# Kernel tuning notes

Hardware: AMD Instinct MI355X
Metric: run time of the kernel (lower is better)

## Reference

```python
import jax, jax.numpy as jnp
import numpy as np

B, S, D = 1024, 200, 512
D_FF = 256


def setup_inputs() -> dict:
    key = jax.random.key(0)
    ks = jax.random.split(key, 8)
    s = 0.02  # init scale to keep gates in a sane range
    return {
        "target": jax.random.normal(ks[0], (B, D), jnp.float32),
        "history": jax.random.normal(ks[1], (B, S, D), jnp.float32),
        "W_ih": jax.random.normal(ks[2], (3 * D, D), jnp.float32) * s,
        "W_hh": jax.random.normal(ks[3], (3 * D, D), jnp.float32) * s,
        "b_ih": jnp.zeros((3 * D,), jnp.float32),
        "b_hh": jnp.zeros((3 * D,), jnp.float32),
        "W_fc": jax.random.normal(ks[4], (D_FF, 2 * D), jnp.float32) * s,
        "b_fc": jnp.zeros((D_FF,), jnp.float32),
        "W_sc": jax.random.normal(ks[5], (1, D_FF), jnp.float32) * s,
        "b_sc": jnp.zeros((1,), jnp.float32),
    }


def _gru(history, W_ih, W_hh, b_ih, b_hh):
    # Precompute input-side gate pre-activations for all steps: [B, S, 3D]
    gx = jnp.einsum("bsd,gd->bsg", history, W_ih) + b_ih
    d = history.shape[-1]
    h0 = jnp.zeros((history.shape[0], d), history.dtype)

    def step(h, gx_t):
        gh = h @ W_hh.T + b_hh  # [B, 3D]
        xr, xz, xn = jnp.split(gx_t, 3, axis=-1)
        hr, hz, hn = jnp.split(gh, 3, axis=-1)
        r = jax.nn.sigmoid(xr + hr)
        z = jax.nn.sigmoid(xz + hz)
        n = jnp.tanh(xn + r * hn)
        h_new = (1.0 - z) * n + z * h
        return h_new, h_new

    _, out = jax.lax.scan(step, h0, jnp.swapaxes(gx, 0, 1))  # out: [S, B, D]
    return jnp.swapaxes(out, 0, 1)  # [B, S, D]


def reference(target, history, W_ih, W_hh, b_ih, b_hh, W_fc, b_fc, W_sc, b_sc):
    d = target.shape[-1]
    gru_out = _gru(history, W_ih, W_hh, b_ih, b_hh)  # [B, S, D]

    # concat([gru_out, target]) @ W_fc.T  == gru_out @ Wg.T + target @ Wt.T
    Wg, Wt = W_fc[:, :d], W_fc[:, d:]
    pre = jnp.einsum("bsd,fd->bsf", gru_out, Wg) + (target @ Wt.T)[:, None, :] + b_fc
    hidden = jax.nn.gelu(pre, approximate=False)  # torch F.gelu default is exact erf
    scores = jnp.einsum("bsf,f->bs", hidden, W_sc[0]) + b_sc[0]  # [B, S]
    w = jax.nn.softmax(scores, axis=-1)
    interest = jnp.einsum("bs,bsd->bd", w, gru_out)  # [B, D]
    return jnp.concatenate([interest, target], axis=-1)  # [B, 2D]
```

## Files before the change

### kernel.cpp

```cpp
#include <hip/hip_runtime.h>

typedef __attribute__((ext_vector_type(8))) short short8v;
typedef __attribute__((ext_vector_type(4))) float f32x4;

#define NB 1024
#define NS 200
#define ND 512
#define NG 1536
#define NM 204800
#define NFF 256

#define GRU_P 4
#define GRU_G 64

__device__ __forceinline__ float bf2f(unsigned short u){
  union { unsigned u; float f; } v; v.u = ((unsigned)u) << 16; return v.f;
}
__device__ __forceinline__ unsigned short f2bf(float f){
  union { float f; unsigned u; } v; v.f = f;
  unsigned r = v.u + 0x7fffu + ((v.u >> 16) & 1u);
  return (unsigned short)(r >> 16);
}
__device__ __forceinline__ float sigm(float x){ return 1.f / (1.f + __expf(-x)); }
__device__ __forceinline__ float tanhfast(float x){ return 1.f - 2.f / (1.f + __expf(2.f * x)); }

__global__ void k_prepack(const float* __restrict__ W, unsigned short* __restrict__ out,
                          int ld, int coloff, int ntiles){
  int gid = blockIdx.x * 256 + threadIdx.x;
  if (gid >= ntiles * 1024) return;
  int ntile = gid >> 10; int rem = gid & 1023;
  int kk = rem >> 6; int lane = rem & 63;
  int c = ntile * 16 + (lane & 15);
  int k0 = kk * 32 + (lane >> 4) * 8;
  const float* s = W + (size_t)c * ld + coloff + k0;
  uint4 v;
  v.x = (unsigned)f2bf(s[0]) | ((unsigned)f2bf(s[1]) << 16);
  v.y = (unsigned)f2bf(s[2]) | ((unsigned)f2bf(s[3]) << 16);
  v.z = (unsigned)f2bf(s[4]) | ((unsigned)f2bf(s[5]) << 16);
  v.w = (unsigned)f2bf(s[6]) | ((unsigned)f2bf(s[7]) << 16);
  *(uint4*)(out + (size_t)gid * 8) = v;
}

__global__ void k_tvec(const float* __restrict__ target, const float* __restrict__ Wfc,
                       const float* __restrict__ bfc, float* __restrict__ tvec){
  __shared__ float tg[4][ND];
  int bb = blockIdx.x;
  int tid = threadIdx.x;
  for (int idx = tid; idx < 4 * ND; idx += 256){
    int j = idx >> 9, d = idx & 511;
    tg[j][d] = target[(size_t)(bb * 4 + j) * ND + d];
  }
  __syncthreads();
  const float* wrow = Wfc + (size_t)tid * 1024 + 512;
  float a0 = 0, a1 = 0, a2 = 0, a3 = 0;
  for (int d = 0; d < ND; ++d){
    float wv = wrow[d];
    a0 += tg[0][d] * wv; a1 += tg[1][d] * wv; a2 += tg[2][d] * wv; a3 += tg[3][d] * wv;
  }
  float bias = bfc[tid];
  tvec[(size_t)(bb * 4 + 0) * NFF + tid] = a0 + bias;
  tvec[(size_t)(bb * 4 + 1) * NFF + tid] = a1 + bias;
  tvec[(size_t)(bb * 4 + 2) * NFF + tid] = a2 + bias;
  tvec[(size_t)(bb * 4 + 3) * NFF + tid] = a3 + bias;
}

__global__ __launch_bounds__(256) void k_gemm_gx(const float* __restrict__ Af,
                                                 const unsigned short* __restrict__ Bpk,
                                                 const float* __restrict__ bih,
                                                 const float* __restrict__ bhh,
                                                 unsigned short* __restrict__ gx){
  __shared__ unsigned short As[128 * 64];
  int tid = threadIdx.x; int lane = tid & 63; int wid = tid >> 6;
  int wm = wid >> 1, wn = wid & 1;
  int Nb = blockIdx.x, Mb = blockIdx.y;
  const float* Abase = Af + (size_t)Mb * 128 * ND;
  const short8v* Bp = (const short8v*)Bpk;
  f32x4 acc[4][4];
  #pragma unroll
  for (int i = 0; i < 4; ++i)
    #pragma unroll
    for (int j = 0; j < 4; ++j) acc[i][j] = (f32x4){0.f, 0.f, 0.f, 0.f};

  for (int kc = 0; kc < 8; ++kc){
    __syncthreads();
    #pragma unroll
    for (int pass = 0; pass < 4; ++pass){
      int idx = pass * 256 + tid; int r = idx >> 3, ch = idx & 7;
      const float* src = Abase + (size_t)r * ND + kc * 64 + ch * 8;
      float4 f0 = *(const float4*)src;
      float4 f1 = *(const float4*)(src + 4);
      uint4 v;
      v.x = (unsigned)f2bf(f0.x) | ((unsigned)f2bf(f0.y) << 16);
      v.y = (unsigned)f2bf(f0.z) | ((unsigned)f2bf(f0.w) << 16);
      v.z = (unsigned)f2bf(f1.x) | ((unsigned)f2bf(f1.y) << 16);
      v.w = (unsigned)f2bf(f1.z) | ((unsigned)f2bf(f1.w) << 16);
      *(uint4*)&As[r * 64 + ch * 8] = v;
    }
    __syncthreads();
    #pragma unroll
    for (int i = 0; i < 2; ++i){
      short8v a[4];
      #pragma unroll
      for (int mt = 0; mt < 4; ++mt)
        a[mt] = *(const short8v*)&As[(wm * 64 + mt * 16 + (lane & 15)) * 64 + i * 32 + (lane >> 4) * 8];
      #pragma unroll
      for (int nt = 0; nt < 4; ++nt){
        short8v b = Bp[((size_t)(Nb * 8 + wn * 4 + nt) * 16 + (kc * 2 + i)) * 64 + lane];
        #pragma unroll
        for (int mt = 0; mt < 4; ++mt)
          acc[mt][nt] = __builtin_amdgcn_mfma_f32_16x16x32_bf16(a[mt], b, acc[mt][nt], 0, 0, 0);
      }
    }
  }
  #pragma unroll
  for (int mt = 0; mt < 4; ++mt){
    #pragma unroll
    for (int nt = 0; nt < 4; ++nt){
      int gcol = Nb * 128 + wn * 64 + nt * 16 + (lane & 15);
      float bv = bih[gcol] + (gcol < 1024 ? bhh[gcol] : 0.f);
      #pragma unroll
      for (int r = 0; r < 4; ++r){
        int grow = Mb * 128 + wm * 64 + mt * 16 + (lane >> 4) * 4 + r;
        gx[(size_t)grow * NG + gcol] = f2bf(acc[mt][nt][r] + bv);
      }
    }
  }
}

__global__ __launch_bounds__(256, 1) void k_gru12(const unsigned short* __restrict__ gx,
                                                  const unsigned short* __restrict__ Wpk,
                                                  const float* __restrict__ bhh,
                                                  unsigned short* __restrict__ gout,
                                                  unsigned long long* __restrict__ hx,
                                                  int* __restrict__ flags){
  __shared__ unsigned short hbuf[2][16 * 512];
  __shared__ unsigned short hstg[16][136];
  int tid = threadIdx.x; int lane = tid & 63; int w = tid >> 6;
  int bid = blockIdx.x; int g = bid & 63; int s = bid >> 6;
  int colg = lane & 15;
  int rowg = lane >> 4;
  int c0 = s * 128 + w * 32 + colg;
  int c1 = c0 + 16;
  int b0 = g * 16;
  int* gfl = flags + g * 16;

  for (int i = tid; i < 16 * 512; i += 256) hbuf[0][i] = 0;

  short8v wf[6][16];
  const short8v* Wp = (const short8v*)Wpk;
  #pragma unroll
  for (int gg = 0; gg < 3; ++gg)
    #pragma unroll
    for (int j = 0; j < 2; ++j){
      int ntile = gg * 32 + s * 8 + w * 2 + j;
      #pragma unroll
      for (int kk = 0; kk < 16; ++kk)
        wf[gg * 2 + j][kk] = Wp[((size_t)ntile * 16 + kk) * 64 + lane];
    }
  float bN0 = bhh[1024 + c0], bN1 = bhh[1024 + c1];
  float hreg[2][4];
  #pragma unroll
  for (int j = 0; j < 2; ++j)
    #pragma unroll
    for (int r = 0; r < 4; ++r) hreg[j][r] = 0.f;

  int wbat = tid >> 4;
  int wc2  = (tid & 15) * 2;

  unsigned short cxr[2][4], cxz[2][4], cxn[2][4];
  #pragma unroll
  for (int r = 0; r < 4; ++r){
    const unsigned short* gp = gx + ((size_t)(b0 + rowg * 4 + r) * NS + 0) * NG;
    cxr[0][r] = gp[c0]; cxz[0][r] = gp[512 + c0]; cxn[0][r] = gp[1024 + c0];
    cxr[1][r] = gp[c1]; cxz[1][r] = gp[512 + c1]; cxn[1][r] = gp[1024 + c1];
  }
  __syncthreads();

  #pragma unroll 1
  for (int t = 0; t < NS; ++t){
    int par = t & 1;
    const unsigned short* hr = hbuf[par];
    f32x4 acc[6];
    #pragma unroll
    for (int nt = 0; nt < 6; ++nt) acc[nt] = (f32x4){0.f, 0.f, 0.f, 0.f};
    #pragma unroll
    for (int kc = 0; kc < 16; ++kc){
      short8v a = *(const short8v*)&hr[kc * 512 + lane * 8];
      #pragma unroll
      for (int nt = 0; nt < 6; ++nt)
        acc[nt] = __builtin_amdgcn_mfma_f32_16x16x32_bf16(a, wf[nt][kc], acc[nt], 0, 0, 0);
    }
    unsigned short hnew[2][4];
    #pragma unroll
    for (int j = 0; j < 2; ++j){
      float bN = j ? bN1 : bN0;
      #pragma unroll
      for (int r = 0; r < 4; ++r){
        float rr = sigm(bf2f(cxr[j][r]) + acc[j][r]);
        float zz = sigm(bf2f(cxz[j][r]) + acc[2 + j][r]);
        float nn = tanhfast(bf2f(cxn[j][r]) + rr * (acc[4 + j][r] + bN));
        float h = nn + zz * (hreg[j][r] - nn);
        hreg[j][r] = h;
        hnew[j][r] = f2bf(h);
      }
    }

    if (t + 1 < NS){
      unsigned long long* hxp = hx + (size_t)par * (1024 * 128);
      #pragma unroll
      for (int j = 0; j < 2; ++j)
        #pragma unroll
        for (int r = 0; r < 4; ++r)
          hstg[rowg * 4 + r][w * 32 + j * 16 + colg] = hnew[j][r];
      __syncthreads();
      {
        unsigned long long v0 = *(const unsigned long long*)&hstg[wbat][wc2 * 4];
        unsigned long long v1 = *(const unsigned long long*)&hstg[wbat][wc2 * 4 + 4];
        __hip_atomic_store(&hxp[(size_t)(b0 + wbat) * 128 + s * 32 + wc2], v0,
                           __ATOMIC_RELAXED, __HIP_MEMORY_SCOPE_AGENT);
        __hip_atomic_store(&hxp[(size_t)(b0 + wbat) * 128 + s * 32 + wc2 + 1], v1,
                           __ATOMIC_RELAXED, __HIP_MEMORY_SCOPE_AGENT);
      }
      asm volatile("s_waitcnt vmcnt(0)" ::: "memory");
      if (lane == 0)
        __hip_atomic_store(&gfl[s * 4 + w], t + 1, __ATOMIC_RELAXED, __HIP_MEMORY_SCOPE_AGENT);
      #pragma unroll
      for (int r = 0; r < 4; ++r){
        unsigned short* gp = gout + ((size_t)(b0 + rowg * 4 + r) * NS + t) * ND;
        gp[c0] = hnew[0][r]; gp[c1] = hnew[1][r];
      }
      #pragma unroll
      for (int r = 0; r < 4; ++r){
        const unsigned short* gp = gx + ((size_t)(b0 + rowg * 4 + r) * NS + (t + 1)) * NG;
        cxr[0][r] = gp[c0]; cxz[0][r] = gp[512 + c0]; cxn[0][r] = gp[1024 + c0];
        cxr[1][r] = gp[c1]; cxz[1][r] = gp[512 + c1]; cxn[1][r] = gp[1024 + c1];
      }
      {
        int need = t + 1; int fv;
        do {
          fv = (lane < 16) ? __hip_atomic_load(&gfl[lane], __ATOMIC_RELAXED, __HIP_MEMORY_SCOPE_AGENT) : need;
        } while (!__all(fv >= need));
      }
      asm volatile("" ::: "memory");
      unsigned short* hw = hbuf[par ^ 1];
      #pragma unroll
      for (int q = 0; q < 4; ++q){
        int kc = w * 4 + q;
        size_t base = (size_t)(b0 + colg) * 128 + kc * 8 + rowg * 2;
        unsigned long long u0 = __hip_atomic_load(&hxp[base],     __ATOMIC_RELAXED, __HIP_MEMORY_SCOPE_AGENT);
        unsigned long long u1 = __hip_atomic_load(&hxp[base + 1], __ATOMIC_RELAXED, __HIP_MEMORY_SCOPE_AGENT);
        unsigned long long tmp[2] = {u0, u1};
        *(uint4*)&hw[kc * 512 + lane * 8] = *(const uint4*)tmp;
      }
      __syncthreads();
    } else {
      #pragma unroll
      for (int r = 0; r < 4; ++r){
        unsigned short* gp = gout + ((size_t)(b0 + rowg * 4 + r) * NS + t) * ND;
        gp[c0] = hnew[0][r]; gp[c1] = hnew[1][r];
      }
    }
  }
}

__global__ __launch_bounds__(512) void k_gemm_s4(const unsigned short* __restrict__ A,
                                                 const unsigned short* __restrict__ Bpk,
                                                 const float* __restrict__ tvec,
                                                 const float* __restrict__ Wsc,
                                                 const float* __restrict__ bsc,
                                                 float* __restrict__ scores){
  __shared__ unsigned short As[128 * 64];
  __shared__ float spart[4][128];
  int tid = threadIdx.x; int lane = tid & 63; int wid = tid >> 6;
  int wm = wid >> 2, wn = wid & 3;
  int Mb = blockIdx.x;
  const unsigned short* Abase = A + (size_t)Mb * 128 * ND;
  const short8v* Bp = (const short8v*)Bpk;
  f32x4 acc[4][4];
  #pragma unroll
  for (int i = 0; i < 4; ++i)
    #pragma unroll
    for (int j = 0; j < 4; ++j) acc[i][j] = (f32x4){0.f, 0.f, 0.f, 0.f};

  for (int kc = 0; kc < 8; ++kc){
    __syncthreads();
    #pragma unroll
    for (int pass = 0; pass < 2; ++pass){
      int idx = pass * 512 + tid; int r = idx >> 3, ch = idx & 7;
      uint4 v = *(const uint4*)(Abase + (size_t)r * ND + kc * 64 + ch * 8);
      *(uint4*)&As[r * 64 + ch * 8] = v;
    }
    __syncthreads();
    #pragma unroll
    for (int i = 0; i < 2; ++i){
      short8v a[4];
      #pragma unroll
      for (int mt = 0; mt < 4; ++mt)
        a[mt] = *(const short8v*)&As[(wm * 64 + mt * 16 + (lane & 15)) * 64 + i * 32 + (lane >> 4) * 8];
      #pragma unroll
      for (int nt = 0; nt < 4; ++nt){
        short8v b = Bp[((size_t)(wn * 4 + nt) * 16 + (kc * 2 + i)) * 64 + lane];
        #pragma unroll
        for (int mt = 0; mt < 4; ++mt)
          acc[mt][nt] = __builtin_amdgcn_mfma_f32_16x16x32_bf16(a[mt], b, acc[mt][nt], 0, 0, 0);
      }
    }
  }
  #pragma unroll
  for (int mt = 0; mt < 4; ++mt){
    #pragma unroll
    for (int r = 0; r < 4; ++r){
      int rowl = wm * 64 + mt * 16 + (lane >> 4) * 4 + r;
      unsigned grow = (unsigned)(Mb * 128 + rowl);
      unsigned bidx = grow / 200u;
      float rowsum = 0.f;
      #pragma unroll
      for (int nt = 0; nt < 4; ++nt){
        int gcol = wn * 64 + nt * 16 + (lane & 15);
        float pre = acc[mt][nt][r] + tvec[(size_t)bidx * NFF + gcol];
        float g = 0.5f * pre * (1.f + erff(pre * 0.70710678118654752f));
        rowsum += g * Wsc[gcol];
      }
      rowsum += __shfl_xor(rowsum, 1, 64);
      rowsum += __shfl_xor(rowsum, 2, 64);
      rowsum += __shfl_xor(rowsum, 4, 64);
      rowsum += __shfl_xor(rowsum, 8, 64);
      if ((lane & 15) == 0) spart[wn][rowl] = rowsum;
    }
  }
  __syncthreads();
  if (tid < 128){
    float s = spart[0][tid] + spart[1][tid] + spart[2][tid] + spart[3][tid] + bsc[0];
    scores[(size_t)Mb * 128 + tid] = s;
  }
}

__global__ void k_out(const float* __restrict__ scores, const unsigned short* __restrict__ gout,
                      const float* __restrict__ target, float* __restrict__ out){
  int b = blockIdx.x; int tid = threadIdx.x;
  __shared__ float sw[NS];
  __shared__ float red[4];
  float v = (tid < NS) ? scores[(size_t)b * NS + tid] : -3.0e38f;
  float m = v;
  #pragma unroll
  for (int off = 32; off >= 1; off >>= 1) m = fmaxf(m, __shfl_xor(m, off, 64));
  if ((tid & 63) == 0) red[tid >> 6] = m;
  __syncthreads();
  m = fmaxf(fmaxf(red[0], red[1]), fmaxf(red[2], red[3]));
  float e = (tid < NS) ? __expf(v - m) : 0.f;
  if (tid < NS) sw[tid] = e;
  float su = e;
  #pragma unroll
  for (int off = 32; off >= 1; off >>= 1) su += __shfl_xor(su, off, 64);
  __syncthreads();
  if ((tid & 63) == 0) red[tid >> 6] = su;
  __syncthreads();
  float inv = 1.f / (red[0] + red[1] + red[2] + red[3]);
  int d0 = tid * 2;
  float a0 = 0.f, a1 = 0.f;
  const unsigned short* gbase = gout + (size_t)b * NS * ND + d0;
  for (int s = 0; s < NS; ++s){
    unsigned u = *(const unsigned*)(gbase + (size_t)s * ND);
    float wgt = sw[s];
    a0 += wgt * bf2f((unsigned short)(u & 0xffffu));
    a1 += wgt * bf2f((unsigned short)(u >> 16));
  }
  out[(size_t)b * 1024 + d0] = a0 * inv;
  out[(size_t)b * 1024 + d0 + 1] = a1 * inv;
  float2 tv = *(const float2*)(target + (size_t)b * ND + d0);
  out[(size_t)b * 1024 + 512 + d0] = tv.x;
  out[(size_t)b * 1024 + 512 + d0 + 1] = tv.y;
}

extern "C" void kernel_launch(void* const* d_in, const int* in_sizes, int n_in,
                              void* d_out, int out_size, void* d_ws, size_t ws_size,
                              hipStream_t stream) {
  const float* target  = (const float*)d_in[0];
  const float* history = (const float*)d_in[1];
  const float* W_ih    = (const float*)d_in[2];
  const float* W_hh    = (const float*)d_in[3];
  const float* b_ih    = (const float*)d_in[4];
  const float* b_hh    = (const float*)d_in[5];
  const float* W_fc    = (const float*)d_in[6];
  const float* b_fc    = (const float*)d_in[7];
  const float* W_sc    = (const float*)d_in[8];
  const float* b_sc    = (const float*)d_in[9];

  char* ws = (char*)d_ws;
  size_t off = 0;
  unsigned short* gx     = (unsigned short*)(ws + off); off += 629145600ull;
  unsigned short* gout   = (unsigned short*)(ws + off); off += 209715200ull;
  unsigned short* wih_pk = (unsigned short*)(ws + off); off += 1572864ull;
  unsigned short* whh_pk = (unsigned short*)(ws + off); off += 1572864ull;
  unsigned short* wg_pk  = (unsigned short*)(ws + off); off += 262144ull;
  float*          tvec   = (float*)(ws + off);          off += 1048576ull;
  float*          scores = (float*)(ws + off);          off += 819200ull;
  unsigned long long* hx = (unsigned long long*)(ws + off); off += 2097152ull;
  int*            flags  = (int*)(ws + off);             off += 4096ull;
  if (ws_size < off) return;
  float* outp = (float*)d_out;

  (void)hipMemsetAsync(flags, 0, GRU_G * 16 * sizeof(int), stream);
  k_prepack<<<384, 256, 0, stream>>>(W_ih, wih_pk, 512, 0, 96);
  k_prepack<<<384, 256, 0, stream>>>(W_hh, whh_pk, 512, 0, 96);
  k_prepack<<<64, 256, 0, stream>>>(W_fc, wg_pk, 1024, 0, 16);
  k_tvec<<<256, 256, 0, stream>>>(target, W_fc, b_fc, tvec);
  k_gemm_gx<<<dim3(12, 1600), 256, 0, stream>>>(history, wih_pk, b_ih, b_hh, gx);
  k_gru12<<<256, 256, 0, stream>>>(gx, whh_pk, b_hh, gout, hx, flags);
  k_gemm_s4<<<1600, 512, 0, stream>>>(gout, wg_pk, tvec, W_sc, b_sc, scores);
  k_out<<<1024, 256, 0, stream>>>(scores, gout, target, outp);
}
```

Measured before the change: 2.084 ms.

## Pre-cast history to bf16 and load GEMM tiles via direct global-to-LDS

```diff
diff --git a/kernel.cpp b/kernel.cpp
--- a/kernel.cpp
+++ b/kernel.cpp
@@ -23,6 +23,27 @@
 }
 __device__ __forceinline__ float sigm(float x){ return 1.f / (1.f + __expf(-x)); }
 __device__ __forceinline__ float tanhfast(float x){ return 1.f - 2.f / (1.f + __expf(2.f * x)); }
+
+__device__ __forceinline__ void gld_lds16(const unsigned short* g, unsigned short* l){
+  __builtin_amdgcn_global_load_lds(
+    (const __attribute__((address_space(1))) unsigned int*)(const void*)g,
+    (__attribute__((address_space(3))) unsigned int*)(void*)l, 16, 0, 0);
+}
+
+__global__ void k_cast_bf16(const float* __restrict__ in, unsigned short* __restrict__ out, size_t n8){
+  size_t i = (size_t)blockIdx.x * blockDim.x + threadIdx.x;
+  size_t stride = (size_t)gridDim.x * blockDim.x;
+  for (; i < n8; i += stride){
+    const float4* p = (const float4*)(in + i * 8);
+    float4 a = p[0], b = p[1];
+    uint4 v;
+    v.x = (unsigned)f2bf(a.x) | ((unsigned)f2bf(a.y) << 16);
+    v.y = (unsigned)f2bf(a.z) | ((unsigned)f2bf(a.w) << 16);
+    v.z = (unsigned)f2bf(b.x) | ((unsigned)f2bf(b.y) << 16);
+    v.w = (unsigned)f2bf(b.z) | ((unsigned)f2bf(b.w) << 16);
+    *(uint4*)(out + i * 8) = v;
+  }
+}
 
 __global__ void k_prepack(const float* __restrict__ W, unsigned short* __restrict__ out,
                           int ld, int coloff, int ntiles){
@@ -64,7 +85,7 @@
   tvec[(size_t)(bb * 4 + 3) * NFF + tid] = a3 + bias;
 }
 
-__global__ __launch_bounds__(256) void k_gemm_gx(const float* __restrict__ Af,
+__global__ __launch_bounds__(256) void k_gemm_gx(const unsigned short* __restrict__ Ab,
                                                  const unsigned short* __restrict__ Bpk,
                                                  const float* __restrict__ bih,
                                                  const float* __restrict__ bhh,
@@ -73,7 +94,7 @@
   int tid = threadIdx.x; int lane = tid & 63; int wid = tid >> 6;
   int wm = wid >> 1, wn = wid & 1;
   int Nb = blockIdx.x, Mb = blockIdx.y;
-  const float* Abase = Af + (size_t)Mb * 128 * ND;
+  const unsigned short* Abase = Ab + (size_t)Mb * 128 * ND;
   const short8v* Bp = (const short8v*)Bpk;
   f32x4 acc[4][4];
   #pragma unroll
@@ -84,18 +105,13 @@
   for (int kc = 0; kc < 8; ++kc){
     __syncthreads();
     #pragma unroll
-    for (int pass = 0; pass < 4; ++pass){
-      int idx = pass * 256 + tid; int r = idx >> 3, ch = idx & 7;
-      const float* src = Abase + (size_t)r * ND + kc * 64 + ch * 8;
-      float4 f0 = *(const float4*)src;
-      float4 f1 = *(const float4*)(src + 4);
-      uint4 v;
-      v.x = (unsigned)f2bf(f0.x) | ((unsigned)f2bf(f0.y) << 16);
-      v.y = (unsigned)f2bf(f0.z) | ((unsigned)f2bf(f0.w) << 16);
-      v.z = (unsigned)f2bf(f1.x) | ((unsigned)f2bf(f1.y) << 16);
-      v.w = (unsigned)f2bf(f1.z) | ((unsigned)f2bf(f1.w) << 16);
-      *(uint4*)&As[r * 64 + ch * 8] = v;
-    }
+    for (int p = 0; p < 4; ++p){
+      int idx = p * 256 + tid; int r = idx >> 3, ch = idx & 7;
+      const unsigned short* src = Abase + (size_t)r * ND + kc * 64 + ch * 8;
+      unsigned short* lb = &As[(size_t)(p * 256 + (tid & ~63)) * 8];
+      gld_lds16(src, lb);
+    }
+    asm volatile("s_waitcnt vmcnt(0)" ::: "memory");
     __syncthreads();
     #pragma unroll
     for (int i = 0; i < 2; ++i){
@@ -318,7 +334,8 @@
       for (int nt = 0; nt < 4; ++nt){
         int gcol = wn * 64 + nt * 16 + (lane & 15);
         float pre = acc[mt][nt][r] + tvec[(size_t)bidx * NFF + gcol];
-        float g = 0.5f * pre * (1.f + erff(pre * 0.70710678118654752f));
+        float p3 = pre * pre * pre;
+        float g = 0.5f * pre * (1.f + tanhfast(0.79788456080286536f * (pre + 0.044715f * p3)));
         rowsum += g * Wsc[gcol];
       }
       rowsum += __shfl_xor(rowsum, 1, 64);
@@ -388,6 +405,7 @@
 
   char* ws = (char*)d_ws;
   size_t off = 0;
+  unsigned short* histb  = (unsigned short*)(ws + off); off += 209715200ull;
   unsigned short* gx     = (unsigned short*)(ws + off); off += 629145600ull;
   unsigned short* gout   = (unsigned short*)(ws + off); off += 209715200ull;
   unsigned short* wih_pk = (unsigned short*)(ws + off); off += 1572864ull;
@@ -401,11 +419,12 @@
   float* outp = (float*)d_out;
 
   (void)hipMemsetAsync(flags, 0, GRU_G * 16 * sizeof(int), stream);
+  k_cast_bf16<<<2048, 256, 0, stream>>>(history, histb, (size_t)13107200ull);
   k_prepack<<<384, 256, 0, stream>>>(W_ih, wih_pk, 512, 0, 96);
   k_prepack<<<384, 256, 0, stream>>>(W_hh, whh_pk, 512, 0, 96);
   k_prepack<<<64, 256, 0, stream>>>(W_fc, wg_pk, 1024, 0, 16);
   k_tvec<<<256, 256, 0, stream>>>(target, W_fc, b_fc, tvec);
-  k_gemm_gx<<<dim3(12, 1600), 256, 0, stream>>>(history, wih_pk, b_ih, b_hh, gx);
+  k_gemm_gx<<<dim3(12, 1600), 256, 0, stream>>>(histb, wih_pk, b_ih, b_hh, gx);
   k_gru12<<<256, 256, 0, stream>>>(gx, whh_pk, b_hh, gout, hx, flags);
   k_gemm_s4<<<1600, 512, 0, stream>>>(gout, wg_pk, tvec, W_sc, b_sc, scores);
   k_out<<<1024, 256, 0, stream>>>(scores, gout, target, outp);
```

Result: faster. 1.992 ms (-4.4%).
